# Optimization experiments

Hardware: AMD Instinct MI355X
Metric: run time of the kernel (lower is better)

The kernel has to match this reference:

```python
import jax, jax.numpy as jnp
import numpy as np

N, K, H = 50000, 8, 128  # nodes per level, mailbox fanout, hidden size


def setup_inputs() -> dict:
    key = jax.random.key(0)
    ks = jax.random.split(key, 16)
    s = 1.0 / np.sqrt(H)
    inp = {
        "x": jax.random.normal(ks[0], (N, H), jnp.float32),
        "h_mail": jax.random.normal(ks[1], (N, K, H), jnp.float32),
        "c_mail": jax.random.normal(ks[2], (N, K, H), jnp.float32),
        "Wiou": jax.random.uniform(ks[3], (H, 3 * H), jnp.float32, -s, s),
        "Uiou": jax.random.uniform(ks[4], (2 * H, 3 * H), jnp.float32, -s, s),
        "biou": jnp.zeros((1, 3 * H), jnp.float32),
        "Of": jax.random.uniform(ks[5], (H, H), jnp.float32, -s, s),
        "Zf": jax.random.uniform(ks[6], (H, H), jnp.float32, -s, s),
        "Qf": jax.random.uniform(ks[7], (H, H), jnp.float32, -s, s),
        "Kf": jax.random.uniform(ks[8], (H, H), jnp.float32, -s, s),
        "vf": jax.random.uniform(ks[9], (H, H), jnp.float32, -s, s),
        "Wa": jax.random.uniform(ks[10], (H, H), jnp.float32, -s, s),
        "Wd": jax.random.uniform(ks[11], (H, H), jnp.float32, -s, s),
        "Vf": jax.random.uniform(ks[12], (H, 1), jnp.float32, -s, s),
        "etype": jax.random.randint(ks[13], (N, K), 0, 2, jnp.int32),
    }
    return inp


def reference(x, h_mail, c_mail, Wiou, Uiou, biou, Of, Zf, Qf, Kf, vf, Wa, Wd, Vf, etype):
    # --- message: mailbox of child h, c and edge type e (0/1) ---
    e = etype.astype(x.dtype)[..., None]                     # [N,K,1]
    # --- reduce_func ---
    x_tild = x @ Wiou                                        # W_iou(features) -> iou  [N,3H]
    n_tild = x @ Qf                                          # [N,H]
    hk = h_mail @ Kf                                         # K_f(h_tild) [N,K,H]
    v_tild = hk @ vf                                         # [N,K,H]
    w = jax.nn.softmax(jnp.tanh((n_tild[:, None, :] + hk) @ Vf), axis=1)  # [N,K,1]
    modify = jnp.mean(e, axis=1)                             # sum(et)/K  [N,1]
    score_a = (1.0 - modify)[:, None, :]                     # [N,1,1]
    score_b = modify[:, None, :]
    h_til1 = jnp.sum(w * score_a * e * (v_tild @ Wa), axis=1)        # [N,H]
    h_til0 = jnp.sum(w * score_b * (1.0 - e) * (v_tild @ Wd), axis=1)
    h_tild = jnp.concatenate([h_til0, h_til1], axis=1)       # [N,2H]
    f = jax.nn.sigmoid((h_mail * e) @ Of + (h_mail * (1.0 - e)) @ Zf)
    c_red = jnp.sum(f * c_mail, axis=1)                      # [N,H]
    iou = h_tild @ Uiou + x_tild                             # [N,3H]
    # --- apply_node_func ---
    iou = iou + biou
    i, o, u = jnp.split(iou, 3, axis=1)
    i, o, u = jax.nn.sigmoid(i), jax.nn.sigmoid(o), jnp.tanh(u)
    c = i * u + c_red
    h = o * jnp.tanh(c)
    return jnp.stack([h, c])                                 # [2,N,H]
```

## Files before the change

kernel.cpp:

```cpp
#include <hip/hip_runtime.h>
#include <math.h>

#define NN 50000
#define HH 128
#define KK 8

#define WS_WTF  0
#define WS_BT   16384
#define WS_KV   90112
#define WS_T0   106496
#define WS_T1   122880
#define WS_kv   139264
#define WS_qv   139392

typedef __attribute__((ext_vector_type(8))) unsigned short u16x8;
typedef __attribute__((ext_vector_type(8))) __bf16 bf16x8;
typedef __attribute__((ext_vector_type(4))) float f32x4;
union Frag { u16x8 u; bf16x8 b; };

__device__ __forceinline__ unsigned short f2bf(float f) {
    unsigned u = __builtin_bit_cast(unsigned, f);
    u += 0x7fffu + ((u >> 16) & 1u);
    return (unsigned short)(u >> 16);
}
__device__ __forceinline__ float sigm(float v) { return 1.f / (1.f + expf(-v)); }

__global__ void prepA(const float* __restrict__ Kf, const float* __restrict__ Qf,
                      const float* __restrict__ vf, const float* __restrict__ Vf,
                      const float* __restrict__ Wiou, const float* __restrict__ Of,
                      const float* __restrict__ Zf, float* __restrict__ ws) {
    int idx = blockIdx.x * 256 + threadIdx.x;
    unsigned short* bt = (unsigned short*)(ws + WS_BT);
    if (idx < 16384) {
        int a = idx >> 7, c = idx & 127;
        float s = 0.f;
        for (int b = 0; b < 128; ++b) s += Kf[a * 128 + b] * vf[b * 128 + c];
        ws[WS_KV + idx] = s;
    } else if (idx < 16512) {
        int a = idx - 16384;
        float s = 0.f;
        for (int b = 0; b < 128; ++b) s += Kf[a * 128 + b] * Vf[b];
        ws[WS_kv + a] = s;
    } else if (idx < 16640) {
        int a = idx - 16512;
        float s = 0.f;
        for (int b = 0; b < 128; ++b) s += Qf[a * 128 + b] * Vf[b];
        ws[WS_qv + a] = s;
    } else if (idx < 65792) {
        int i = idx - 16640;
        int r = i / 384, c = i % 384;
        bt[c * 384 + r] = f2bf(Wiou[i]);
    } else {
        int i = idx - 65792;
        int c = i >> 8, k = i & 255;
        float v = (k < 128) ? Of[k * 128 + c] : Zf[(k - 128) * 128 + c];
        unsigned short* wtf = (unsigned short*)(ws + WS_WTF);
        wtf[i] = f2bf(v);
    }
}

__global__ void prep2(const float* __restrict__ Wd, const float* __restrict__ Wa,
                      float* __restrict__ ws) {
    int idx = blockIdx.x * 256 + threadIdx.x;
    int sel = idx >> 14;
    int r = (idx >> 7) & 127, c = idx & 127;
    const float* W = sel ? Wa : Wd;
    const float* Kv = ws + WS_KV;
    float s = 0.f;
    for (int h = 0; h < 128; ++h) s += Kv[r * 128 + h] * W[h * 128 + c];
    ws[(sel ? WS_T1 : WS_T0) + r * 128 + c] = s;
}

__global__ void prep3(const float* __restrict__ Uiou, float* __restrict__ ws) {
    int idx = blockIdx.x * 256 + threadIdx.x;
    int half = (idx >= 49152) ? 1 : 0;
    int i2 = idx - half * 49152;
    int r = i2 / 384, c = i2 % 384;
    const float* T = ws + (half ? WS_T1 : WS_T0);
    const float* U = Uiou + half * 128 * 384;
    float s = 0.f;
    for (int h = 0; h < 128; ++h) s += T[r * 128 + h] * U[h * 384 + c];
    unsigned short* bt = (unsigned short*)(ws + WS_BT);
    bt[c * 384 + (128 + half * 128 + r)] = f2bf(s);
}

__global__ __launch_bounds__(256, 4) void tree_main(
    const float* __restrict__ x, const float* __restrict__ h_mail,
    const float* __restrict__ c_mail, const float* __restrict__ biou,
    const int* __restrict__ etype, const float* __restrict__ ws,
    float* __restrict__ out)
{
    __shared__ unsigned short GfS[48 * 128];
    __shared__ float credS[16 * 132];
    __shared__ float efS[128];
    __shared__ float kvqS[256];

    const int t = threadIdx.x;
    const int node0 = blockIdx.x * 16;

    {
        const int n = t >> 4, s = t & 15, c0 = s * 8;
        const int node = node0 + n;
        kvqS[t] = ws[WS_kv + t];
        if (t < 128) efS[t] = (float)etype[node0 * KK + t];

        float xv[8];
        const float4* xp = (const float4*)(x + node * HH + c0);
        float4 x0 = xp[0], x1 = xp[1];
        xv[0]=x0.x; xv[1]=x0.y; xv[2]=x0.z; xv[3]=x0.w;
        xv[4]=x1.x; xv[5]=x1.y; xv[6]=x1.z; xv[7]=x1.w;
        u16x8 xg;
        #pragma unroll
        for (int j = 0; j < 8; ++j) xg[j] = f2bf(xv[j]);
        *(u16x8*)(&GfS[s * 128 + n * 8]) = xg;
        __syncthreads();

        float xq = 0.f;
        #pragma unroll
        for (int j = 0; j < 8; ++j) xq += xv[j] * kvqS[128 + c0 + j];

        float hv[KK][8];
        float p[KK];
        #pragma unroll
        for (int k = 0; k < KK; ++k) {
            const float4* hp = (const float4*)(h_mail + (node * KK + k) * HH + c0);
            float4 h0 = hp[0], h1 = hp[1];
            hv[k][0]=h0.x; hv[k][1]=h0.y; hv[k][2]=h0.z; hv[k][3]=h0.w;
            hv[k][4]=h1.x; hv[k][5]=h1.y; hv[k][6]=h1.z; hv[k][7]=h1.w;
            float pk = 0.f;
            #pragma unroll
            for (int j = 0; j < 8; ++j) pk += hv[k][j] * kvqS[c0 + j];
            p[k] = pk;
        }
        #pragma unroll
        for (int msk = 8; msk >= 1; msk >>= 1) {
            xq += __shfl_xor(xq, msk, 16);
            #pragma unroll
            for (int k = 0; k < KK; ++k) p[k] += __shfl_xor(p[k], msk, 16);
        }
        float ef[KK], esum = 0.f;
        #pragma unroll
        for (int k = 0; k < KK; ++k) { ef[k] = efS[n * KK + k]; esum += ef[k]; }
        const float mod = esum * 0.125f;
        const float sa = 1.f - mod, sb = mod;

        float tk[KK], mx = -1e30f;
        #pragma unroll
        for (int k = 0; k < KK; ++k) { tk[k] = tanhf(xq + p[k]); mx = fmaxf(mx, tk[k]); }
        float wsum = 0.f;
        #pragma unroll
        for (int k = 0; k < KK; ++k) { tk[k] = expf(tk[k] - mx); wsum += tk[k]; }
        const float inv = 1.f / wsum;
        float a0[8] = {0,0,0,0,0,0,0,0}, a1[8] = {0,0,0,0,0,0,0,0};
        #pragma unroll
        for (int k = 0; k < KK; ++k) {
            float w = tk[k] * inv;
            const float cf0 = sb * w * (1.f - ef[k]);
            const float cf1 = sa * w * ef[k];
            #pragma unroll
            for (int j = 0; j < 8; ++j) { a0[j] += cf0 * hv[k][j]; a1[j] += cf1 * hv[k][j]; }
        }
        u16x8 g0, g1;
        #pragma unroll
        for (int j = 0; j < 8; ++j) { g0[j] = f2bf(a0[j]); g1[j] = f2bf(a1[j]); }
        *(u16x8*)(&GfS[(16 + s) * 128 + n * 8]) = g0;
        *(u16x8*)(&GfS[(32 + s) * 128 + n * 8]) = g1;
    }
    __syncthreads();

    const int wave = t >> 6, lane = t & 63, m = lane & 15, q = lane >> 4;
    {
        const unsigned short* WtF = (const unsigned short*)(ws + WS_WTF);
        f32x4 acc[2][8];
        #pragma unroll
        for (int rt = 0; rt < 2; ++rt)
            #pragma unroll
            for (int tc = 0; tc < 8; ++tc) acc[rt][tc] = (f32x4){0.f,0.f,0.f,0.f};

        #pragma unroll
        for (int ks = 0; ks < 8; ++ks) {
            const int kg = ks * 32 + q * 8;
            Frag bf[8], af[2];
            #pragma unroll
            for (int tc = 0; tc < 8; ++tc)
                bf[tc].u = *(const u16x8*)(WtF + (tc * 16 + m) * 256 + kg);
            #pragma unroll
            for (int rt = 0; rt < 2; ++rt) {
                const int r = wave * 32 + rt * 16 + m;
                const float msk = (ks < 4) ? efS[r] : (1.f - efS[r]);
                const float4* hp = (const float4*)(h_mail + (node0 * KK + r) * HH + (kg & 127));
                float4 h0 = hp[0], h1 = hp[1];
                float tv[8];
                tv[0]=h0.x*msk; tv[1]=h0.y*msk; tv[2]=h0.z*msk; tv[3]=h0.w*msk;
                tv[4]=h1.x*msk; tv[5]=h1.y*msk; tv[6]=h1.z*msk; tv[7]=h1.w*msk;
                #pragma unroll
                for (int j = 0; j < 8; ++j) af[rt].u[j] = f2bf(tv[j]);
            }
            #pragma unroll
            for (int rt = 0; rt < 2; ++rt)
                #pragma unroll
                for (int tc = 0; tc < 8; ++tc)
                    acc[rt][tc] = __builtin_amdgcn_mfma_f32_16x16x32_bf16(
                        af[rt].b, bf[tc].b, acc[rt][tc], 0, 0, 0);
        }
        #pragma unroll
        for (int rt = 0; rt < 2; ++rt) {
            const int rbase = wave * 32 + rt * 16;
            const float* cp = c_mail + (node0 * KK + rbase + q * 4) * HH + m;
            float cm[8][4];
            #pragma unroll
            for (int tc = 0; tc < 8; ++tc)
                #pragma unroll
                for (int reg = 0; reg < 4; ++reg)
                    cm[tc][reg] = cp[reg * HH + tc * 16];
            #pragma unroll
            for (int tc = 0; tc < 8; ++tc) {
                float sacc = 0.f;
                #pragma unroll
                for (int reg = 0; reg < 4; ++reg)
                    sacc += sigm(acc[rt][tc][reg]) * cm[tc][reg];
                sacc += __shfl_xor(sacc, 16);
                if ((q & 1) == 0) {
                    const int nl = (rbase >> 3) + (q >> 1);
                    credS[nl * 132 + tc * 16 + m] = sacc;
                }
            }
        }
    }

    f32x4 acc2[6];
    {
        const unsigned short* Bt = (const unsigned short*)(ws + WS_BT);
        #pragma unroll
        for (int j = 0; j < 6; ++j) acc2[j] = (f32x4){0.f,0.f,0.f,0.f};
        #pragma unroll
        for (int ks = 0; ks < 12; ++ks) {
            const int kg = ks * 32 + q * 8;
            Frag ag;
            ag.u = *(const u16x8*)(&GfS[(kg >> 3) * 128 + m * 8]);
            #pragma unroll
            for (int j = 0; j < 6; ++j) {
                const int tile = (j >> 1) * 8 + wave * 2 + (j & 1);
                Frag bg;
                bg.u = *(const u16x8*)(Bt + (tile * 16 + m) * 384 + kg);
                acc2[j] = __builtin_amdgcn_mfma_f32_16x16x32_bf16(
                    ag.b, bg.b, acc2[j], 0, 0, 0);
            }
        }
    }
    __syncthreads();

    {
        #pragma unroll
        for (int jj = 0; jj < 2; ++jj) {
            const int c = (wave * 2 + jj) * 16 + m;
            const float bi = biou[c];
            const float bo = biou[128 + c];
            const float bu = biou[256 + c];
            #pragma unroll
            for (int reg = 0; reg < 4; ++reg) {
                const int n = q * 4 + reg;
                const float ii = sigm(acc2[jj][reg] + bi);
                const float oo = sigm(acc2[2 + jj][reg] + bo);
                const float uu = tanhf(acc2[4 + jj][reg] + bu);
                const float cc = ii * uu + credS[n * 132 + c];
                out[(node0 + n) * HH + c] = oo * tanhf(cc);
                out[NN * HH + (node0 + n) * HH + c] = cc;
            }
        }
    }
}

extern "C" void kernel_launch(void* const* d_in, const int* in_sizes, int n_in,
                              void* d_out, int out_size, void* d_ws, size_t ws_size,
                              hipStream_t stream) {
    const float* x      = (const float*)d_in[0];
    const float* h_mail = (const float*)d_in[1];
    const float* c_mail = (const float*)d_in[2];
    const float* Uiou   = (const float*)d_in[4];
    const float* biou   = (const float*)d_in[5];
    const float* Of     = (const float*)d_in[6];
    const float* Zf     = (const float*)d_in[7];
    const float* Qf     = (const float*)d_in[8];
    const float* Kf     = (const float*)d_in[9];
    const float* vf     = (const float*)d_in[10];
    const float* Wa     = (const float*)d_in[11];
    const float* Wd     = (const float*)d_in[12];
    const float* Vf     = (const float*)d_in[13];
    const int*   etype  = (const int*)d_in[14];
    const float* Wiou   = (const float*)d_in[3];
    float* ws  = (float*)d_ws;
    float* out = (float*)d_out;

    hipLaunchKernelGGL(prepA, dim3(385), dim3(256), 0, stream, Kf, Qf, vf, Vf, Wiou, Of, Zf, ws);
    hipLaunchKernelGGL(prep2, dim3(128), dim3(256), 0, stream, Wd, Wa, ws);
    hipLaunchKernelGGL(prep3, dim3(384), dim3(256), 0, stream, Uiou, ws);
    hipLaunchKernelGGL(tree_main, dim3(3125), dim3(256), 0, stream,
                       x, h_mail, c_mail, biou, etype, ws, out);
}
```

Measured before the change: 847.7 us.

## Swizzle GfS LDS layout, reload h_mail instead of caching, drop kvq LDS

The change XOR-swizzles the GfS shared-memory layout to reduce bank conflicts on the 16-byte stores and fragment reads. It stops holding the 8x8 h_mail values in registers and instead reloads them from global memory (likely L1/L2 hits) for the weighted accumulation. The kv/qv vectors now come straight from global memory, not shared memory. It also pins waves-per-EU to 4. Together these aim to cut VGPR pressure and LDS conflicts, at the cost of a second pass of global loads over h_mail.

```diff
diff --git a/kernel.cpp b/kernel.cpp
--- a/kernel.cpp
+++ b/kernel.cpp
@@ -24,6 +24,8 @@
     return (unsigned short)(u >> 16);
 }
 __device__ __forceinline__ float sigm(float v) { return 1.f / (1.f + expf(-v)); }
+
+#define GF(row, slot) ((row) * 128 + ((((slot) ^ ((row) & 7))) << 3))
 
 __global__ void prepA(const float* __restrict__ Kf, const float* __restrict__ Qf,
                       const float* __restrict__ vf, const float* __restrict__ Vf,
@@ -84,7 +86,8 @@
     bt[c * 384 + (128 + half * 128 + r)] = f2bf(s);
 }
 
-__global__ __launch_bounds__(256, 4) void tree_main(
+__global__ __launch_bounds__(256) __attribute__((amdgpu_waves_per_eu(4, 4)))
+void tree_main(
     const float* __restrict__ x, const float* __restrict__ h_mail,
     const float* __restrict__ c_mail, const float* __restrict__ biou,
     const int* __restrict__ etype, const float* __restrict__ ws,
@@ -93,7 +96,6 @@
     __shared__ unsigned short GfS[48 * 128];
     __shared__ float credS[16 * 132];
     __shared__ float efS[128];
-    __shared__ float kvqS[256];
 
     const int t = threadIdx.x;
     const int node0 = blockIdx.x * 16;
@@ -101,7 +103,6 @@
     {
         const int n = t >> 4, s = t & 15, c0 = s * 8;
         const int node = node0 + n;
-        kvqS[t] = ws[WS_kv + t];
         if (t < 128) efS[t] = (float)etype[node0 * KK + t];
 
         float xv[8];
@@ -112,25 +113,27 @@
         u16x8 xg;
         #pragma unroll
         for (int j = 0; j < 8; ++j) xg[j] = f2bf(xv[j]);
-        *(u16x8*)(&GfS[s * 128 + n * 8]) = xg;
+        *(u16x8*)(&GfS[GF(s, n)]) = xg;
+
+        const float4* kvp = (const float4*)(ws + WS_kv + c0);
+        float4 k0 = kvp[0], k1 = kvp[1];
+        const float4* qvp = (const float4*)(ws + WS_qv + c0);
+        float4 q0 = qvp[0], q1 = qvp[1];
+        float kvv[8] = {k0.x,k0.y,k0.z,k0.w,k1.x,k1.y,k1.z,k1.w};
+        float qvv[8] = {q0.x,q0.y,q0.z,q0.w,q1.x,q1.y,q1.z,q1.w};
         __syncthreads();
 
         float xq = 0.f;
         #pragma unroll
-        for (int j = 0; j < 8; ++j) xq += xv[j] * kvqS[128 + c0 + j];
-
-        float hv[KK][8];
+        for (int j = 0; j < 8; ++j) xq += xv[j] * qvv[j];
+
         float p[KK];
         #pragma unroll
         for (int k = 0; k < KK; ++k) {
             const float4* hp = (const float4*)(h_mail + (node * KK + k) * HH + c0);
             float4 h0 = hp[0], h1 = hp[1];
-            hv[k][0]=h0.x; hv[k][1]=h0.y; hv[k][2]=h0.z; hv[k][3]=h0.w;
-            hv[k][4]=h1.x; hv[k][5]=h1.y; hv[k][6]=h1.z; hv[k][7]=h1.w;
-            float pk = 0.f;
-            #pragma unroll
-            for (int j = 0; j < 8; ++j) pk += hv[k][j] * kvqS[c0 + j];
-            p[k] = pk;
+            p[k] = h0.x*kvv[0] + h0.y*kvv[1] + h0.z*kvv[2] + h0.w*kvv[3]
+                 + h1.x*kvv[4] + h1.y*kvv[5] + h1.z*kvv[6] + h1.w*kvv[7];
         }
         #pragma unroll
         for (int msk = 8; msk >= 1; msk >>= 1) {
@@ -151,20 +154,29 @@
         #pragma unroll
         for (int k = 0; k < KK; ++k) { tk[k] = expf(tk[k] - mx); wsum += tk[k]; }
         const float inv = 1.f / wsum;
-        float a0[8] = {0,0,0,0,0,0,0,0}, a1[8] = {0,0,0,0,0,0,0,0};
+        float cf0[KK], cf1[KK];
         #pragma unroll
         for (int k = 0; k < KK; ++k) {
             float w = tk[k] * inv;
-            const float cf0 = sb * w * (1.f - ef[k]);
-            const float cf1 = sa * w * ef[k];
-            #pragma unroll
-            for (int j = 0; j < 8; ++j) { a0[j] += cf0 * hv[k][j]; a1[j] += cf1 * hv[k][j]; }
+            cf0[k] = sb * w * (1.f - ef[k]);
+            cf1[k] = sa * w * ef[k];
+        }
+        float a0[8] = {0,0,0,0,0,0,0,0}, a1[8] = {0,0,0,0,0,0,0,0};
+        #pragma unroll
+        for (int k = 0; k < KK; ++k) {
+            const float4* hp = (const float4*)(h_mail + (node * KK + k) * HH + c0);
+            float4 h0 = hp[0], h1 = hp[1];
+            float hv[8];
+            hv[0]=h0.x; hv[1]=h0.y; hv[2]=h0.z; hv[3]=h0.w;
+            hv[4]=h1.x; hv[5]=h1.y; hv[6]=h1.z; hv[7]=h1.w;
+            #pragma unroll
+            for (int j = 0; j < 8; ++j) { a0[j] += cf0[k]*hv[j]; a1[j] += cf1[k]*hv[j]; }
         }
         u16x8 g0, g1;
         #pragma unroll
         for (int j = 0; j < 8; ++j) { g0[j] = f2bf(a0[j]); g1[j] = f2bf(a1[j]); }
-        *(u16x8*)(&GfS[(16 + s) * 128 + n * 8]) = g0;
-        *(u16x8*)(&GfS[(32 + s) * 128 + n * 8]) = g1;
+        *(u16x8*)(&GfS[GF(16 + s, n)]) = g0;
+        *(u16x8*)(&GfS[GF(32 + s, n)]) = g1;
     }
     __syncthreads();
 
@@ -236,8 +248,9 @@
         #pragma unroll
         for (int ks = 0; ks < 12; ++ks) {
             const int kg = ks * 32 + q * 8;
+            const int row = kg >> 3;
             Frag ag;
-            ag.u = *(const u16x8*)(&GfS[(kg >> 3) * 128 + m * 8]);
+            ag.u = *(const u16x8*)(&GfS[GF(row, m)]);
             #pragma unroll
             for (int j = 0; j < 6; ++j) {
                 const int tile = (j >> 1) * 8 + wave * 2 + (j & 1);
```

Result: slower. 884.1 us (+4.3%).
